# Performance work log

Measured on AMD Instinct MI355X. Metric: run time of the kernel, lower is better.

Reference implementation:

```python
import jax, jax.numpy as jnp
import numpy as np
from jax import lax

D_MODEL = 512; N_HEADS = 32; HEAD_DIM = 16
D_INNER = 1024; D_STATE = 64; HDIM = 64; NH = 16; D_CONV = 4
CONV_CH = D_INNER + 2 * D_STATE          # 1152
D_INPROJ = 2 * D_INNER + 2 * D_STATE + NH  # 2192
B, L = 4, 1024


def setup_inputs() -> dict:
    key = jax.random.key(0)
    ks = jax.random.split(key, 16)
    def rn(k, shape, scale=0.02):
        return jax.random.normal(k, shape, jnp.float32) * scale
    inp = {"h": jax.random.normal(ks[0], (B, L, D_MODEL), jnp.float32)}
    inp["attn_in_w"] = rn(ks[1], (3 * D_MODEL, D_MODEL))
    inp["attn_in_b"] = jnp.zeros((3 * D_MODEL,), jnp.float32)
    inp["attn_out_w"] = rn(ks[2], (D_MODEL, D_MODEL))
    inp["attn_out_b"] = jnp.zeros((D_MODEL,), jnp.float32)
    i = 3
    for p in ("fwd", "bwd"):
        inp[f"{p}_inproj_w"] = rn(ks[i], (D_INPROJ, D_MODEL)); i += 1
        inp[f"{p}_conv_w"] = rn(ks[i], (CONV_CH, D_CONV), 0.1); i += 1
        inp[f"{p}_conv_b"] = jnp.zeros((CONV_CH,), jnp.float32)
        inp[f"{p}_dt_bias"] = rn(ks[i], (NH,), 0.5); i += 1
        inp[f"{p}_A_log"] = jnp.log(jax.random.uniform(ks[i], (NH,), jnp.float32, 1.0, 16.0)); i += 1
        inp[f"{p}_D"] = jnp.ones((NH,), jnp.float32)
        inp[f"{p}_norm_w"] = jnp.ones((D_INNER,), jnp.float32)
        inp[f"{p}_outproj_w"] = rn(ks[i], (D_MODEL, D_INNER)); i += 1
    inp["ln_w"] = jnp.ones((D_MODEL,), jnp.float32)
    inp["ln_b"] = jnp.zeros((D_MODEL,), jnp.float32)
    return inp


def _mha(h, in_w, in_b, out_w, out_b):
    b, l, d = h.shape
    qkv = h @ in_w.T + in_b
    q, k, v = jnp.split(qkv, 3, axis=-1)
    def heads(t):
        return t.reshape(b, l, N_HEADS, HEAD_DIM).transpose(0, 2, 1, 3)
    q, k, v = heads(q), heads(k), heads(v)
    scores = jnp.einsum('bhqd,bhkd->bhqk', q, k) * (1.0 / np.sqrt(HEAD_DIM))
    attn = jax.nn.softmax(scores, axis=-1)
    o = jnp.einsum('bhqk,bhkd->bhqd', attn, v).transpose(0, 2, 1, 3).reshape(b, l, d)
    return o @ out_w.T + out_b


def _causal_dwconv(x, w, bias):
    # x: (b, l, c), w: (c, k) depthwise causal conv
    xt = x.transpose(0, 2, 1)  # (b, c, l)
    out = lax.conv_general_dilated(xt, w[:, None, :], (1,), [(D_CONV - 1, 0)],
                                   feature_group_count=CONV_CH,
                                   dimension_numbers=('NCH', 'OIH', 'NCH'))
    return (out + bias[None, :, None]).transpose(0, 2, 1)


def _ssd(x, dt, A, Bm, Cm):
    # x: (b,l,nh,p), dt: (b,l,nh), Bm/Cm: (b,l,n) (ngroups=1)
    b = x.shape[0]
    dA = jnp.exp(dt * A)          # (b,l,nh)
    dtx = dt[..., None] * x       # (b,l,nh,p)
    def step(hst, inp):
        dA_t, dtx_t, B_t, C_t = inp
        hst = dA_t[:, :, None, None] * hst + dtx_t[..., None] * B_t[:, None, None, :]
        return hst, jnp.einsum('bhpn,bn->bhp', hst, C_t)
    init = jnp.zeros((b, NH, HDIM, D_STATE), x.dtype)
    _, ys = lax.scan(step, init, (dA.transpose(1, 0, 2), dtx.transpose(1, 0, 2, 3),
                                  Bm.transpose(1, 0, 2), Cm.transpose(1, 0, 2)))
    return ys.transpose(1, 0, 2, 3)  # (b,l,nh,p)


def _mamba2(u, inproj_w, conv_w, conv_b, dt_bias, A_log, Dp, norm_w, outproj_w):
    b, l, _ = u.shape
    zxbcdt = u @ inproj_w.T                      # (b,l,2192)
    z = zxbcdt[..., :D_INNER]
    xBC = zxbcdt[..., D_INNER:D_INNER + CONV_CH]
    dt = jax.nn.softplus(zxbcdt[..., D_INNER + CONV_CH:] + dt_bias)  # (b,l,nh)
    xBC = jax.nn.silu(_causal_dwconv(xBC, conv_w, conv_b))
    x = xBC[..., :D_INNER].reshape(b, l, NH, HDIM)
    Bm = xBC[..., D_INNER:D_INNER + D_STATE]
    Cm = xBC[..., D_INNER + D_STATE:]
    A = -jnp.exp(A_log)
    y = _ssd(x, dt, A, Bm, Cm) + Dp[None, None, :, None] * x
    y = y.reshape(b, l, D_INNER) * jax.nn.silu(z)  # gated (norm_before_gate=False)
    y = y * lax.rsqrt(jnp.mean(y * y, axis=-1, keepdims=True) + 1e-5) * norm_w  # RMSNormGated
    return y @ outproj_w.T


def reference(h, attn_in_w, attn_in_b, attn_out_w, attn_out_b,
              fwd_inproj_w, fwd_conv_w, fwd_conv_b, fwd_dt_bias, fwd_A_log, fwd_D, fwd_norm_w, fwd_outproj_w,
              bwd_inproj_w, bwd_conv_w, bwd_conv_b, bwd_dt_bias, bwd_A_log, bwd_D, bwd_norm_w, bwd_outproj_w,
              ln_w, ln_b):
    attn_out = _mha(h, attn_in_w, attn_in_b, attn_out_w, attn_out_b)
    fwd_out = _mamba2(h, fwd_inproj_w, fwd_conv_w, fwd_conv_b, fwd_dt_bias, fwd_A_log, fwd_D, fwd_norm_w, fwd_outproj_w)
    bwd_out = jnp.flip(_mamba2(jnp.flip(h, 1), bwd_inproj_w, bwd_conv_w, bwd_conv_b, bwd_dt_bias, bwd_A_log, bwd_D, bwd_norm_w, bwd_outproj_w), 1)
    s = h + attn_out + fwd_out + bwd_out
    mu = jnp.mean(s, axis=-1, keepdims=True)
    var = jnp.mean((s - mu) ** 2, axis=-1, keepdims=True)
    return (s - mu) * lax.rsqrt(var + 1e-5) * ln_w + ln_b
```

## Files before the change

kernel.cpp:

```cpp
#include <hip/hip_runtime.h>
#include <math.h>
#include <stdint.h>

#define B_ 4
#define L_ 1024
#define DM 512
#define NHA 32
#define HD 16
#define DI 1024
#define DSTATE 64
#define HDIM_ 64
#define NHM 16
#define DCONV 4
#define CONVCH 1152
#define DINPROJ 2192
#define NTOK (B_*L_)
#define QC 64
#define NC (L_/QC)
#define QKVS 5920

typedef __bf16 bf16x8 __attribute__((ext_vector_type(8)));
typedef float f32x4 __attribute__((ext_vector_type(4)));
typedef unsigned short ushort8 __attribute__((ext_vector_type(8)));
typedef unsigned short ushort4v __attribute__((ext_vector_type(4)));
typedef __fp16 fp16x2 __attribute__((ext_vector_type(2)));
typedef _Float16 f16x4 __attribute__((ext_vector_type(4)));
typedef _Float16 f16x8 __attribute__((ext_vector_type(8)));

__device__ __forceinline__ float siluf(float x) {
    return x / (1.0f + __expf(-x));
}

__device__ __forceinline__ unsigned short f2bf(float f) {
    unsigned u = __float_as_uint(f);
    unsigned r = (u + 0x7FFFu + ((u >> 16) & 1u)) >> 16;
    return (unsigned short)r;
}

__device__ __forceinline__ float bf2f(unsigned short u) {
    return __uint_as_float((unsigned)u << 16);
}

__device__ __forceinline__ void cvt8(const float* src, unsigned short* dst) {
    float4 a = ((const float4*)src)[0];
    float4 b = ((const float4*)src)[1];
    ushort8 o;
    o[0] = f2bf(a.x); o[1] = f2bf(a.y); o[2] = f2bf(a.z); o[3] = f2bf(a.w);
    o[4] = f2bf(b.x); o[5] = f2bf(b.y); o[6] = f2bf(b.z); o[7] = f2bf(b.w);
    *(ushort8*)dst = o;
}

__device__ __forceinline__ void gload16(const void* g, void* l) {
    auto gp = reinterpret_cast<const __attribute__((address_space(1))) unsigned int*>(
        reinterpret_cast<uintptr_t>(g));
    auto lp = reinterpret_cast<__attribute__((address_space(3))) unsigned int*>(
        reinterpret_cast<uintptr_t>(l));
    __builtin_amdgcn_global_load_lds(gp, lp, 16, 0, 0);
}

#define S0 262144
#define S1 (S0 + 98304)
#define S2 (S1 + 32768)
#define S3 (S2 + 140288)
#define S4 (S3 + 140288)
__global__ void cvt_all_kernel(const float* __restrict__ h, unsigned short* __restrict__ hB,
                               const float* __restrict__ w1, unsigned short* __restrict__ d1,
                               const float* __restrict__ w2, unsigned short* __restrict__ d2,
                               const float* __restrict__ w3, unsigned short* __restrict__ d3,
                               const float* __restrict__ w4, unsigned short* __restrict__ d4) {
    int i = blockIdx.x * blockDim.x + threadIdx.x;
    const float* src; unsigned short* dst; int off;
    if (i < S0)      { src = h;  dst = hB; off = i; }
    else if (i < S1) { src = w1; dst = d1; off = i - S0; }
    else if (i < S2) { src = w2; dst = d2; off = i - S1; }
    else if (i < S3) { src = w3; dst = d3; off = i - S2; }
    else             { src = w4; dst = d4; off = i - S3; }
    cvt8(src + (size_t)off * 8, dst + (size_t)off * 8);
}

__global__ void cvt_outproj_kernel(const float* __restrict__ fw, const float* __restrict__ bw,
                                   unsigned short* __restrict__ dst) {
    int i = blockIdx.x * blockDim.x + threadIdx.x;
    const int n8 = DM * DI / 8;
    int half = i >= n8;
    int off = half ? i - n8 : i;
    const float* src = half ? bw : fw;
    int e = off * 8;
    int r = e / DI, c = e % DI;
    cvt8(src + e, dst + (size_t)r * 2048 + half * 1024 + c);
}

template <int BN, bool OBF16, bool SWZ>
__global__ __launch_bounds__(256) void gemm_mfma_staged(
        const unsigned short* __restrict__ Ab, const unsigned short* __restrict__ Wb,
        const float* __restrict__ bias, int biasN, void* __restrict__ Cout,
        int M, int N, int K) {
    constexpr int BM = 128, BK = 32;
    constexpr int NF = BN / 32;
    constexpr int BLOADS = BN / 64;
    __shared__ unsigned short As[2][BM * BK];
    __shared__ unsigned short Bs[2][BN * BK];

    const int tid = threadIdx.x;
    const int wave = tid >> 6, lane = tid & 63;
    const int l15 = lane & 15, g = lane >> 4;
    const int wm = wave >> 1, wn = wave & 1;
    int m0, n0;
    if constexpr (SWZ) {
        int d = blockIdx.x;
        int xcd = d & 7, jj = d >> 3;
        n0 = (xcd * 6 + jj % 6) * BN;
        m0 = (jj / 6) * BM;
    } else {
        m0 = blockIdx.y * BM;
        n0 = blockIdx.x * BN;
    }

    f32x4 acc[4][NF];
    #pragma unroll
    for (int mi = 0; mi < 4; ++mi)
        #pragma unroll
        for (int nj = 0; nj < NF; ++nj) acc[mi][nj] = (f32x4){0.f, 0.f, 0.f, 0.f};

    auto stage = [&](int bufi, int k0) {
        #pragma unroll
        for (int i = 0; i < 2; ++i) {
            int c = (wave * 2 + i) * 64 + lane;
            int row = c >> 2;
            int kc = ((c & 3) ^ (row & 3)) * 8;
            gload16(Ab + (size_t)(m0 + row) * K + k0 + kc,
                    &As[bufi][(wave * 2 + i) * 64 * 8]);
        }
        #pragma unroll
        for (int i = 0; i < BLOADS; ++i) {
            int c = (wave * BLOADS + i) * 64 + lane;
            int row = c >> 2;
            int kc = ((c & 3) ^ (row & 3)) * 8;
            int rn = n0 + row; if (rn >= N) rn = N - 1;
            gload16(Wb + (size_t)rn * K + k0 + kc,
                    &Bs[bufi][(wave * BLOADS + i) * 64 * 8]);
        }
    };

    int cur = 0;
    stage(0, 0);
    __syncthreads();
    for (int k0 = 0; k0 < K; k0 += BK) {
        if (k0 + BK < K) stage(cur ^ 1, k0 + BK);
        const unsigned short* Ac = As[cur];
        const unsigned short* Bc = Bs[cur];
        bf16x8 af[4];
        #pragma unroll
        for (int mi = 0; mi < 4; ++mi) {
            int ar = wm * 64 + mi * 16 + l15;
            af[mi] = *(const bf16x8*)(Ac + ar * BK + ((g ^ (ar & 3)) * 8));
        }
        bf16x8 bfr[NF];
        #pragma unroll
        for (int nj = 0; nj < NF; ++nj) {
            int br = wn * (BN / 2) + nj * 16 + l15;
            bfr[nj] = *(const bf16x8*)(Bc + br * BK + ((g ^ (br & 3)) * 8));
        }
        #pragma unroll
        for (int mi = 0; mi < 4; ++mi)
            #pragma unroll
            for (int nj = 0; nj < NF; ++nj)
                acc[mi][nj] = __builtin_amdgcn_mfma_f32_16x16x32_bf16(af[mi], bfr[nj], acc[mi][nj], 0, 0, 0);
        __syncthreads();
        cur ^= 1;
    }

    #pragma unroll
    for (int mi = 0; mi < 4; ++mi) {
        int rbase = m0 + wm * 64 + mi * 16 + g * 4;
        #pragma unroll
        for (int nj = 0; nj < NF; ++nj) {
            int col = n0 + wn * (BN / 2) + nj * 16 + l15;
            if (col < N) {
                float bv = (bias && col < biasN) ? bias[col] : 0.f;
                #pragma unroll
                for (int r = 0; r < 4; ++r) {
                    float v = acc[mi][nj][r] + bv;
                    if constexpr (OBF16)
                        ((unsigned short*)Cout)[(size_t)(rbase + r) * N + col] = f2bf(v);
                    else
                        ((float*)Cout)[(size_t)(rbase + r) * N + col] = v;
                }
            }
        }
    }
}

#define PBAR() do { __builtin_amdgcn_sched_barrier(0); __builtin_amdgcn_s_barrier(); } while (0)
#define MMAQ(MI0, BP, NJ0)                                                                   \
    do {                                                                                     \
        __builtin_amdgcn_s_setprio(1);                                                       \
        _Pragma("unroll")                                                                    \
        for (int i_ = 0; i_ < 4; ++i_) {                                                     \
            _Pragma("unroll")                                                                \
            for (int j_ = 0; j_ < 2; ++j_) {                                                 \
                acc[(MI0)+i_][(NJ0)+j_] = __builtin_amdgcn_mfma_f32_16x16x32_bf16(           \
                    af[i_][0], BP[j_][0], acc[(MI0)+i_][(NJ0)+j_], 0, 0, 0);                 \
                acc[(MI0)+i_][(NJ0)+j_] = __builtin_amdgcn_mfma_f32_16x16x32_bf16(           \
                    af[i_][1], BP[j_][1], acc[(MI0)+i_][(NJ0)+j_], 0, 0, 0);                 \
            }                                                                                \
        }                                                                                    \
        __builtin_amdgcn_s_setprio(0);                                                       \
    } while (0)

__global__ __launch_bounds__(512, 2) void gemm_mega_8phase(
        const unsigned short* __restrict__ Ab, const unsigned short* __restrict__ Wb,
        const float* __restrict__ bias, int biasN, unsigned short* __restrict__ Cout,
        int M, int Nreal, int K) {
    extern __shared__ unsigned short lds[];
    unsigned short* const LA = lds;
    unsigned short* const LB = lds + 4 * 8192;

    const int tid = threadIdx.x;
    const int wave = tid >> 6, lane = tid & 63;
    const int l15 = lane & 15, g4 = lane >> 4;
    const int wm = wave >> 2, wn = wave & 3;

    const int wg = blockIdx.x;
    const int lin = (wg & 7) * 48 + (wg >> 3);
    const int m0 = (lin & 15) * 256;
    const int n0 = (lin >> 4) * 256;

    f32x4 acc[8][4];
    #pragma unroll
    for (int i = 0; i < 8; ++i)
        #pragma unroll
        for (int j = 0; j < 4; ++j) acc[i][j] = (f32x4){0.f, 0.f, 0.f, 0.f};

    auto stA = [&](int buf, int half, int kt) {
        #pragma unroll
        for (int i2 = 0; i2 < 2; ++i2) {
            int c = (wave * 2 + i2) * 64 + lane;
            int row = c >> 3, ch = c & 7;
            gload16(Ab + (size_t)(m0 + half * 128 + row) * K + kt * 64 + ((ch ^ (row & 7)) * 8),
                    LA + (buf * 2 + half) * 8192 + (wave * 2 + i2) * 512);
        }
    };
    auto stB = [&](int buf, int half, int kt) {
        #pragma unroll
        for (int i2 = 0; i2 < 2; ++i2) {
            int c = (wave * 2 + i2) * 64 + lane;
            int row = c >> 3, ch = c & 7;
            int rn = n0 + half * 128 + row;
            if (rn >= Nreal) rn = Nreal - 1;
            gload16(Wb + (size_t)rn * K + kt * 64 + ((ch ^ (row & 7)) * 8),
                    LB + (buf * 2 + half) * 8192 + (wave * 2 + i2) * 512);
        }
    };

    bf16x8 af[4][2], b01[2][2], b23[2][2];

    auto ldA = [&](int buf, int miBase) {
        #pragma unroll
        for (int i = 0; i < 4; ++i) {
            int r = (miBase + i) * 16 + l15;
            #pragma unroll
            for (int ks = 0; ks < 2; ++ks) {
                int ch = ks * 4 + g4;
                af[i][ks] = *(const bf16x8*)(LA + (buf * 2 + wm) * 8192 + r * 64 +
                                             ((ch ^ (r & 7)) * 8));
            }
        }
    };
    auto ldB = [&](int buf, int njBase, bf16x8 (&bp)[2][2]) {
        #pragma unroll
        for (int j = 0; j < 2; ++j) {
            int r = (wn & 1) * 64 + (njBase + j) * 16 + l15;
            #pragma unroll
            for (int ks = 0; ks < 2; ++ks) {
                int ch = ks * 4 + g4;
                bp[j][ks] = *(const bf16x8*)(LB + (buf * 2 + (wn >> 1)) * 8192 + r * 64 +
                                             ((ch ^ (r & 7)) * 8));
            }
        }
    };

    stA(0, 0, 0); stA(0, 1, 0); stB(0, 0, 0); stB(0, 1, 0);
    stB(1, 0, 1); stB(1, 1, 1);
    asm volatile("s_waitcnt vmcnt(4)" ::: "memory");
    PBAR();

    const int NIT = K >> 7;
    for (int it = 0; it < NIT; ++it) {
        const int T1 = 2 * it + 1;
        const bool st = (it + 1 < NIT);
        ldA(0, 0); ldB(0, 0, b01);
        stA(1, 0, T1);
        PBAR();
        MMAQ(0, b01, 0);
        PBAR();
        ldB(0, 2, b23);
        stA(1, 1, T1);
        PBAR();
        MMAQ(0, b23, 2);
        PBAR();
        ldA(0, 4);
        if (st) stB(0, 0, T1 + 1);
        PBAR();
        MMAQ(4, b23, 2);
        PBAR();
        if (st) {
            stB(0, 1, T1 + 1);
            asm volatile("s_waitcnt vmcnt(4)" ::: "memory");
        } else {
            asm volatile("s_waitcnt vmcnt(0)" ::: "memory");
        }
        PBAR();
        MMAQ(4, b01, 0);
        PBAR();
        ldA(1, 0); ldB(1, 0, b01);
        if (st) stA(0, 0, T1 + 1);
        PBAR();
        MMAQ(0, b01, 0);
        PBAR();
        ldB(1, 2, b23);
        if (st) stA(0, 1, T1 + 1);
        PBAR();
        MMAQ(0, b23, 2);
        PBAR();
        ldA(1, 4);
        if (st) stB(1, 0, T1 + 2);
        PBAR();
        MMAQ(4, b23, 2);
        PBAR();
        if (st) {
            stB(1, 1, T1 + 2);
            asm volatile("s_waitcnt vmcnt(4)" ::: "memory");
        }
        PBAR();
        MMAQ(4, b01, 0);
        PBAR();
    }

    #pragma unroll
    for (int mi = 0; mi < 8; ++mi) {
        int rbase = m0 + wm * 128 + mi * 16 + g4 * 4;
        #pragma unroll
        for (int nj = 0; nj < 4; ++nj) {
            int col = n0 + wn * 64 + nj * 16 + l15;
            if (col < Nreal) {
                float bv = (col < biasN) ? bias[col] : 0.f;
                #pragma unroll
                for (int r = 0; r < 4; ++r)
                    Cout[(size_t)(rbase + r) * Nreal + col] = f2bf(acc[mi][nj][r] + bv);
            }
        }
    }
}

#define KP 24
#define VP 132
__global__ __launch_bounds__(256) void attn_mfma_kernel(const unsigned short* __restrict__ qkv,
                                                        unsigned short* __restrict__ ob) {
    const int n = blockIdx.x;
    const int xcd = n & 7;
    const int j = n >> 3;
    const int bh = ((j >> 4) << 3) + xcd;
    const int qt = j & 15;
    const int h = bh & 31;
    const int b = bh >> 5;
    const int tid = threadIdx.x;
    const int wave = tid >> 6, lane = tid & 63;
    const int l15 = lane & 15, g = lane >> 4;

    __shared__ _Float16 Ksm[128 * KP];
    __shared__ _Float16 VsmT[16 * VP];

    const unsigned short* base = qkv + (size_t)b * L_ * QKVS;
    const int qrow = qt * 64 + wave * 16 + l15;

    f16x4 qf;
    {
        ushort4v qv = *(const ushort4v*)(base + (size_t)qrow * QKVS + h * 16 + g * 4);
        fp16x2 qa = __builtin_amdgcn_cvt_pkrtz(bf2f(qv[0]) * 0.25f, bf2f(qv[1]) * 0.25f);
        fp16x2 qb = __builtin_amdgcn_cvt_pkrtz(bf2f(qv[2]) * 0.25f, bf2f(qv[3]) * 0.25f);
        qf[0] = (_Float16)qa[0]; qf[1] = (_Float16)qa[1];
        qf[2] = (_Float16)qb[0]; qf[3] = (_Float16)qb[1];
    }
    f32x4 yacc = (f32x4){0.f, 0.f, 0.f, 0.f};
    float s = 0.f;

    const int sk = tid >> 1;
    const int sd = (tid & 1) * 8;

    for (int c0 = 0; c0 < L_; c0 += 128) {
        {
            ushort8 ka = *(const ushort8*)(base + (size_t)(c0 + sk) * QKVS + 512 + h * 16 + sd);
            fp16x2 k0 = __builtin_amdgcn_cvt_pkrtz(bf2f(ka[0]), bf2f(ka[1]));
            fp16x2 k1 = __builtin_amdgcn_cvt_pkrtz(bf2f(ka[2]), bf2f(ka[3]));
            fp16x2 k2 = __builtin_amdgcn_cvt_pkrtz(bf2f(ka[4]), bf2f(ka[5]));
            fp16x2 k3 = __builtin_amdgcn_cvt_pkrtz(bf2f(ka[6]), bf2f(ka[7]));
            f16x8 kv;
            kv[0] = (_Float16)k0[0]; kv[1] = (_Float16)k0[1];
            kv[2] = (_Float16)k1[0]; kv[3] = (_Float16)k1[1];
            kv[4] = (_Float16)k2[0]; kv[5] = (_Float16)k2[1];
            kv[6] = (_Float16)k3[0]; kv[7] = (_Float16)k3[1];
            *(f16x8*)(&Ksm[sk * KP + sd]) = kv;
            ushort8 va = *(const ushort8*)(base + (size_t)(c0 + sk) * QKVS + 1024 + h * 16 + sd);
            #pragma unroll
            for (int jj = 0; jj < 8; ++jj)
                VsmT[(sd + jj) * VP + sk] = (_Float16)bf2f(va[jj]);
        }
        __syncthreads();
        #pragma unroll
        for (int half = 0; half < 2; ++half) {
            f32x4 st[4];
            #pragma unroll
            for (int ks = 0; ks < 4; ++ks) {
                f16x4 kf = *(const f16x4*)(&Ksm[((half * 4 + ks) * 16 + l15) * KP + g * 4]);
                st[ks] = __builtin_amdgcn_mfma_f32_16x16x16f16(kf, qf, (f32x4){0.f,0.f,0.f,0.f}, 0, 0, 0);
            }
            float p[16];
            float cs = 0.f;
            #pragma unroll
            for (int ks = 0; ks < 4; ++ks) {
                #pragma unroll
                for (int r = 0; r < 4; ++r) {
                    p[ks * 4 + r] = __expf(st[ks][r]);
                    cs += p[ks * 4 + r];
                }
            }
            cs += __shfl_xor(cs, 16);
            cs += __shfl_xor(cs, 32);
            s += cs;
            #pragma unroll
            for (int ks = 0; ks < 4; ++ks) {
                fp16x2 plo = __builtin_amdgcn_cvt_pkrtz(p[ks*4+0], p[ks*4+1]);
                fp16x2 phi = __builtin_amdgcn_cvt_pkrtz(p[ks*4+2], p[ks*4+3]);
                f16x4 pf;
                pf[0] = (_Float16)plo[0]; pf[1] = (_Float16)plo[1];
                pf[2] = (_Float16)phi[0]; pf[3] = (_Float16)phi[1];
                f16x4 vf = *(const f16x4*)(&VsmT[l15 * VP + (half * 4 + ks) * 16 + g * 4]);
                yacc = __builtin_amdgcn_mfma_f32_16x16x16f16(vf, pf, yacc, 0, 0, 0);
            }
        }
        __syncthreads();
    }
    float inv = 1.f / s;
    ushort4v o;
    o[0] = f2bf(yacc[0] * inv);
    o[1] = f2bf(yacc[1] * inv);
    o[2] = f2bf(yacc[2] * inv);
    o[3] = f2bf(yacc[3] * inv);
    *(ushort4v*)(ob + (size_t)(b * L_ + qrow) * 512 + h * 16 + g * 4) = o;
}

__global__ void conv_silu_kernel(const unsigned short* __restrict__ megaA,
                                 const float* __restrict__ cw0, const float* __restrict__ cb0,
                                 const float* __restrict__ cw1, const float* __restrict__ cb1,
                                 unsigned short* __restrict__ out) {
    const int rev = blockIdx.y;
    const float* conv_w = rev ? cw1 : cw0;
    const float* conv_b = rev ? cb1 : cb0;
    int idx = blockIdx.x * blockDim.x + threadIdx.x;
    if (idx >= NTOK * (CONVCH / 4)) return;
    int c4 = (idx % (CONVCH / 4)) * 4;
    int bl = idx / (CONVCH / 4);
    int l = bl % L_;
    int b = bl / L_;
    const unsigned short* src = megaA + (size_t)b * L_ * QKVS + 1536 + rev * DINPROJ + 1024 + c4;
    float4 w0 = *(const float4*)(conv_w + (c4 + 0) * 4);
    float4 w1 = *(const float4*)(conv_w + (c4 + 1) * 4);
    float4 w2 = *(const float4*)(conv_w + (c4 + 2) * 4);
    float4 w3 = *(const float4*)(conv_w + (c4 + 3) * 4);
    float4 acc = *(const float4*)(conv_b + c4);
    const float wt[4][4] = {{w0.x, w0.y, w0.z, w0.w}, {w1.x, w1.y, w1.z, w1.w},
                            {w2.x, w2.y, w2.z, w2.w}, {w3.x, w3.y, w3.z, w3.w}};
    #pragma unroll
    for (int j = 0; j < 4; ++j) {
        int ll = rev ? (l + 3 - j) : (l - 3 + j);
        if (ll >= 0 && ll < L_) {
            ushort4v x = *(const ushort4v*)(src + (size_t)ll * QKVS);
            acc.x = fmaf(wt[0][j], bf2f(x[0]), acc.x);
            acc.y = fmaf(wt[1][j], bf2f(x[1]), acc.y);
            acc.z = fmaf(wt[2][j], bf2f(x[2]), acc.z);
            acc.w = fmaf(wt[3][j], bf2f(x[3]), acc.w);
        }
    }
    ushort4v o;
    o[0] = f2bf(siluf(acc.x)); o[1] = f2bf(siluf(acc.y));
    o[2] = f2bf(siluf(acc.z)); o[3] = f2bf(siluf(acc.w));
    *(ushort4v*)(out + (size_t)rev * NTOK * CONVCH + (size_t)bl * CONVCH + c4) = o;
}

__global__ void dt_exact_kernel(const float* __restrict__ h,
                                const float* __restrict__ wdt0, const float* __restrict__ bias0,
                                const float* __restrict__ wdt1, const float* __restrict__ bias1,
                                float* __restrict__ dt) {
    const int dir = blockIdx.y;
    const float* wdt = dir ? wdt1 : wdt0;
    const float* dbias = dir ? bias1 : bias0;
    const int row = blockIdx.x;
    const int tid = threadIdx.x;
    const int g = tid >> 4, j = tid & 15;
    const float* hr = h + (size_t)row * DM;
    const float* wr = wdt + (size_t)g * DM;
    float s = 0.f;
    #pragma unroll 8
    for (int t = 0; t < 32; ++t) {
        int k = j + t * 16;
        s = fmaf(hr[k], wr[k], s);
    }
    s += __shfl_xor(s, 1); s += __shfl_xor(s, 2);
    s += __shfl_xor(s, 4); s += __shfl_xor(s, 8);
    if (j == 0) {
        float v = s + dbias[g];
        dt[(size_t)dir * NTOK * NHM + (size_t)row * NHM + g] = (v > 20.f) ? v : log1pf(__expf(v));
    }
}

__global__ __launch_bounds__(256) void ssd_chunk_kernel(
        const unsigned short* __restrict__ xbcAll, const float* __restrict__ dtAll,
        const float* __restrict__ Al0, const float* __restrict__ Dp0,
        const float* __restrict__ Al1, const float* __restrict__ Dp1,
        unsigned short* __restrict__ y16, float* __restrict__ Sb0, float* __restrict__ Sb1,
        float* __restrict__ Edec) {
    const int dir = blockIdx.y;
    const int rev = dir;
    const unsigned short* xbc = xbcAll + (size_t)dir * NTOK * CONVCH;
    const float* dtb = dtAll + (size_t)dir * NTOK * NHM;
    float* Sbuf = dir ? Sb1 : Sb0;
    unsigned short* y = y16 + (size_t)dir * NTOK * DI;

    const int bid = blockIdx.x;
    const int q = bid & (NC - 1);
    const int bh = bid / NC;
    const int b = bh >> 4, h = bh & 15;
    const int tid = threadIdx.x;
    const int wave = tid >> 6, lane = tid & 63;
    const int l15 = lane & 15, l4 = lane >> 4;

    __shared__ unsigned short Bn[64 * 72];
    __shared__ unsigned short Cn[64 * 72];
    __shared__ unsigned short Btw[64 * 72];
    __shared__ unsigned short Gt[64 * 72];
    __shared__ unsigned short xT[64 * 72];
    __shared__ float sdt[QC], sc[QC], wsv[QC];

    const float A = -__expf((dir ? Al1 : Al0)[h]);
    const float Dh = (dir ? Dp1 : Dp0)[h];
    const int r = tid >> 2, qq = tid & 3;

    #pragma unroll
    for (int j = 0; j < 4; ++j) {
        int qd = qq + j * 4;
        int t = q * QC + r;
        int l = rev ? (L_ - 1 - t) : t;
        const unsigned short* rowp = xbc + (size_t)(b * L_ + l) * CONVCH;
        *(ushort4v*)&Bn[r * 72 + qd * 4] = *(const ushort4v*)(rowp + 1024 + qd * 4);
        *(ushort4v*)&Cn[r * 72 + qd * 4] = *(const ushort4v*)(rowp + 1088 + qd * 4);
    }
    if (tid < QC) {
        int t = q * QC + tid;
        int l = rev ? (L_ - 1 - t) : t;
        sdt[tid] = dtb[(size_t)(b * L_ + l) * NHM + h];
    }
    __syncthreads();
    if (tid == 0) {
        float run = 0.f;
        for (int i = 0; i < QC; ++i) { run += A * sdt[i]; sc[i] = run; }
    }
    __syncthreads();
    if (tid < QC) wsv[tid] = sdt[tid] * __expf(sc[QC - 1] - sc[tid]);
    if (tid == 0) Edec[dir * 1024 + bid] = __expf(sc[QC - 1]);
    __syncthreads();

    {
        int n = tid >> 2, s0 = (tid & 3) * 16;
        ushort8 o0, o1;
        #pragma unroll
        for (int k = 0; k < 8; ++k) {
            o0[k] = f2bf(bf2f(Bn[(s0 + k) * 72 + n]) * wsv[s0 + k]);
            o1[k] = f2bf(bf2f(Bn[(s0 + 8 + k) * 72 + n]) * wsv[s0 + 8 + k]);
        }
        *(ushort8*)&Btw[n * 72 + s0] = o0;
        *(ushort8*)&Btw[n * 72 + s0 + 8] = o1;
    }
    #pragma unroll
    for (int j = 0; j < 4; ++j) {
        int qd = qq + j * 4;
        int t = q * QC + r;
        int l = rev ? (L_ - 1 - t) : t;
        const unsigned short* rowp = xbc + (size_t)(b * L_ + l) * CONVCH + h * 64;
        ushort4v xv = *(const ushort4v*)(rowp + qd * 4);
        xT[(qd * 4 + 0) * 72 + r] = xv[0];
        xT[(qd * 4 + 1) * 72 + r] = xv[1];
        xT[(qd * 4 + 2) * 72 + r] = xv[2];
        xT[(qd * 4 + 3) * 72 + r] = xv[3];
    }
    __syncthreads();

    f32x4 accG[4];
    #pragma unroll
    for (int j = 0; j < 4; ++j) accG[j] = (f32x4){0.f, 0.f, 0.f, 0.f};
    #pragma unroll
    for (int k0 = 0; k0 < 64; k0 += 32) {
        bf16x8 af = *(const bf16x8*)&Bn[(wave * 16 + l15) * 72 + l4 * 8 + k0];
        #pragma unroll
        for (int j = 0; j < 4; ++j) {
            bf16x8 bfj = *(const bf16x8*)&Cn[(j * 16 + l15) * 72 + l4 * 8 + k0];
            accG[j] = __builtin_amdgcn_mfma_f32_16x16x32_bf16(af, bfj, accG[j], 0, 0, 0);
        }
    }
    #pragma unroll
    for (int j = 0; j < 4; ++j) {
        #pragma unroll
        for (int rr = 0; rr < 4; ++rr) {
            int s = wave * 16 + l4 * 4 + rr;
            int i = j * 16 + l15;
            float g = (s <= i) ? accG[j][rr] * sdt[s] * __expf(sc[i] - sc[s]) : 0.f;
            Gt[i * 72 + s] = f2bf(g);
        }
    }
    __syncthreads();

    {
        f32x4 accY[4];
        #pragma unroll
        for (int j = 0; j < 4; ++j) accY[j] = (f32x4){0.f, 0.f, 0.f, 0.f};
        #pragma unroll
        for (int k0 = 0; k0 < 64; k0 += 32) {
            bf16x8 af = *(const bf16x8*)&Gt[(wave * 16 + l15) * 72 + l4 * 8 + k0];
            #pragma unroll
            for (int j = 0; j < 4; ++j) {
                bf16x8 bfj = *(const bf16x8*)&xT[(j * 16 + l15) * 72 + l4 * 8 + k0];
                accY[j] = __builtin_amdgcn_mfma_f32_16x16x32_bf16(af, bfj, accY[j], 0, 0, 0);
            }
        }
        #pragma unroll
        for (int j = 0; j < 4; ++j) {
            #pragma unroll
            for (int rr = 0; rr < 4; ++rr) {
                int i = wave * 16 + l4 * 4 + rr;
                int p = j * 16 + l15;
                int t = q * QC + i;
                int l = rev ? (L_ - 1 - t) : t;
                float xv = bf2f(xT[p * 72 + i]);
                y[(size_t)(b * L_ + l) * DI + h * 64 + p] = f2bf(accY[j][rr] + Dh * xv);
            }
        }
    }
    {
        f32x4 accS[4];
        #pragma unroll
        for (int j = 0; j < 4; ++j) accS[j] = (f32x4){0.f, 0.f, 0.f, 0.f};
        #pragma unroll
        for (int k0 = 0; k0 < 64; k0 += 32) {
            bf16x8 af = *(const bf16x8*)&xT[(wave * 16 + l15) * 72 + l4 * 8 + k0];
            #pragma unroll
            for (int j = 0; j < 4; ++j) {
                bf16x8 bfj = *(const bf16x8*)&Btw[(j * 16 + l15) * 72 + l4 * 8 + k0];
                accS[j] = __builtin_amdgcn_mfma_f32_16x16x32_bf16(af, bfj, accS[j], 0, 0, 0);
            }
        }
        float* Sq = Sbuf + (size_t)bid * 4096;
        #pragma unroll
        for (int j = 0; j < 4; ++j) {
            #pragma unroll
            for (int rr = 0; rr < 4; ++rr) {
                int p = wave * 16 + l4 * 4 + rr;
                int n = j * 16 + l15;
                Sq[p * 64 + n] = accS[j][rr];
            }
        }
    }
}

__global__ void ssd_chain_kernel(float* __restrict__ Sb0, float* __restrict__ Sb1,
                                 const float* __restrict__ Edec) {
    const int dir = blockIdx.z;
    float* Sbuf = dir ? Sb1 : Sb0;
    const int bh = blockIdx.x;
    const int e = blockIdx.y * 256 + threadIdx.x;
    float* base = Sbuf + (size_t)bh * NC * 4096 + e;
    const float* Ep = Edec + dir * 1024 + bh * NC;
    float hst = 0.f;
    float tmp = base[0];
    #pragma unroll
    for (int q = 0; q < NC; ++q) {
        float nxt = (q + 1 < NC) ? base[(size_t)(q + 1) * 4096] : 0.f;
        float E = Ep[q];
        base[(size_t)q * 4096] = hst;
        hst = fmaf(E, hst, tmp);
        tmp = nxt;
    }
}

__global__ __launch_bounds__(256) void ssd_corr_kernel(
        const unsigned short* __restrict__ xbcAll, const float* __restrict__ dtAll,
        const float* __restrict__ Al0, const float* __restrict__ Al1,
        const float* __restrict__ Sb0, const float* __restrict__ Sb1,
        unsigned short* __restrict__ y16) {
    const int dir = blockIdx.y;
    const int rev = dir;
    const unsigned short* xbc = xbcAll + (size_t)dir * NTOK * CONVCH;
    const float* dtb = dtAll + (size_t)dir * NTOK * NHM;
    const float* Sbuf = dir ? Sb1 : Sb0;
    unsigned short* y = y16 + (size_t)dir * NTOK * DI;

    const int bid = blockIdx.x;
    const int q = bid & (NC - 1);
    const int bh = bid / NC;
    const int b = bh >> 4, h = bh & 15;
    const int tid = threadIdx.x;
    const int wave = tid >> 6, lane = tid & 63;
    const int l15 = lane & 15, l4 = lane >> 4;

    __shared__ unsigned short Cb[64 * 72];
    __shared__ unsigned short Hb[64 * 72];
    __shared__ float sdt[QC], sc[QC];
    const float A = -__expf((dir ? Al1 : Al0)[h]);
    const int r = tid >> 2, qq = tid & 3;
    const float* Sq = Sbuf + (size_t)bid * 4096;

    #pragma unroll
    for (int j = 0; j < 4; ++j) {
        int qd = qq + j * 4;
        int t = q * QC + r;
        int l = rev ? (L_ - 1 - t) : t;
        const unsigned short* rowp = xbc + (size_t)(b * L_ + l) * CONVCH;
        *(ushort4v*)&Cb[r * 72 + qd * 4] = *(const ushort4v*)(rowp + 1088 + qd * 4);
        float4 hv = ((const float4*)Sq)[r * 16 + qd];
        ushort4v hh;
        hh[0] = f2bf(hv.x); hh[1] = f2bf(hv.y); hh[2] = f2bf(hv.z); hh[3] = f2bf(hv.w);
        *(ushort4v*)&Hb[r * 72 + qd * 4] = hh;
    }
    if (tid < QC) {
        int t = q * QC + tid;
        int l = rev ? (L_ - 1 - t) : t;
        sdt[tid] = dtb[(size_t)(b * L_ + l) * NHM + h];
    }
    __syncthreads();
    if (tid == 0) {
        float run = 0.f;
        for (int i = 0; i < QC; ++i) { run += A * sdt[i]; sc[i] = run; }
    }
    __syncthreads();

    f32x4 acc[4];
    #pragma unroll
    for (int j = 0; j < 4; ++j) acc[j] = (f32x4){0.f, 0.f, 0.f, 0.f};
    #pragma unroll
    for (int k0 = 0; k0 < 64; k0 += 32) {
        bf16x8 af = *(const bf16x8*)&Cb[(wave * 16 + l15) * 72 + l4 * 8 + k0];
        #pragma unroll
        for (int j = 0; j < 4; ++j) {
            bf16x8 bfj = *(const bf16x8*)&Hb[(j * 16 + l15) * 72 + l4 * 8 + k0];
            acc[j] = __builtin_amdgcn_mfma_f32_16x16x32_bf16(af, bfj, acc[j], 0, 0, 0);
        }
    }
    #pragma unroll
    for (int j = 0; j < 4; ++j) {
        #pragma unroll
        for (int rr = 0; rr < 4; ++rr) {
            int i = wave * 16 + l4 * 4 + rr;
            int p = j * 16 + l15;
            int t = q * QC + i;
            int l = rev ? (L_ - 1 - t) : t;
            float e = __expf(sc[i]);
            unsigned short* yp = &y[(size_t)(b * L_ + l) * DI + h * 64 + p];
            *yp = f2bf(bf2f(*yp) + e * acc[j][rr]);
        }
    }
}

__global__ void gate_rmsnorm_kernel(const unsigned short* __restrict__ y16,
                                    const unsigned short* __restrict__ megaA,
                                    const float* __restrict__ nw0, const float* __restrict__ nw1,
                                    unsigned short* __restrict__ yb) {
    const int dir = blockIdx.y;
    const float* norm_w = dir ? nw1 : nw0;
    const int row = blockIdx.x;
    const int tid = threadIdx.x;
    const unsigned short* z = megaA + (size_t)row * QKVS + 1536 + dir * DINPROJ;
    const unsigned short* yr = y16 + (size_t)dir * NTOK * DI + (size_t)row * DI;
    float v[4];
    float ss = 0.f;
    #pragma unroll
    for (int i = 0; i < 4; ++i) {
        int c = i * 256 + tid;
        float g = siluf(bf2f(z[c]));
        v[i] = bf2f(yr[c]) * g;
        ss = fmaf(v[i], v[i], ss);
    }
    #pragma unroll
    for (int off = 32; off > 0; off >>= 1) ss += __shfl_xor(ss, off);
    __shared__ float red[4];
    int wid = tid >> 6, lane = tid & 63;
    if (lane == 0) red[wid] = ss;
    __syncthreads();
    ss = red[0] + red[1] + red[2] + red[3];
    float scale = rsqrtf(ss * (1.0f / 1024.0f) + 1e-5f);
    #pragma unroll
    for (int i = 0; i < 4; ++i) {
        int c = i * 256 + tid;
        yb[(size_t)row * 2048 + dir * 1024 + c] = f2bf(v[i] * scale * norm_w[c]);
    }
}

__global__ void final_ln_kernel(const float* __restrict__ h, const float* __restrict__ attn,
                                const float* __restrict__ msum,
                                const float* __restrict__ ln_w, const float* __restrict__ ln_b,
                                float* __restrict__ out) {
    const int row = blockIdx.x;
    const int tid = threadIdx.x;
    size_t base = (size_t)row * DM;
    float v[2];
    float sum = 0.f, sq = 0.f;
    #pragma unroll
    for (int i = 0; i < 2; ++i) {
        int c = i * 256 + tid;
        float s = h[base + c] + attn[base + c] + msum[base + c];
        v[i] = s;
        sum += s;
        sq = fmaf(s, s, sq);
    }
    #pragma unroll
    for (int off = 32; off > 0; off >>= 1) {
        sum += __shfl_xor(sum, off);
        sq += __shfl_xor(sq, off);
    }
    __shared__ float rsum[4], rsq[4];
    int wid = tid >> 6, lane = tid & 63;
    if (lane == 0) { rsum[wid] = sum; rsq[wid] = sq; }
    __syncthreads();
    sum = rsum[0] + rsum[1] + rsum[2] + rsum[3];
    sq = rsq[0] + rsq[1] + rsq[2] + rsq[3];
    float mu = sum * (1.0f / DM);
    float var = sq * (1.0f / DM) - mu * mu;
    float rs = rsqrtf(var + 1e-5f);
    #pragma unroll
    for (int i = 0; i < 2; ++i) {
        int c = i * 256 + tid;
        out[base + c] = (v[i] - mu) * rs * ln_w[c] + ln_b[c];
    }
}

extern "C" void kernel_launch(void* const* d_in, const int* in_sizes, int n_in,
                              void* d_out, int out_size, void* d_ws, size_t ws_size,
                              hipStream_t stream) {
    const float* h          = (const float*)d_in[0];
    const float* attn_in_w  = (const float*)d_in[1];
    const float* attn_in_b  = (const float*)d_in[2];
    const float* attn_out_w = (const float*)d_in[3];
    const float* attn_out_b = (const float*)d_in[4];
    const float* ln_w       = (const float*)d_in[21];
    const float* ln_b       = (const float*)d_in[22];
    float* out = (float*)d_out;

    float* ws = (float*)d_ws;
    unsigned short* megaA = (unsigned short*)ws;
    unsigned short* bufXBC = (unsigned short*)(ws + 12124160);
    float* bufDT   = ws + 12124160 + 4718592;
    float* bufY    = bufDT + 131072;
    float* bufATTN = bufY + 4194304;
    float* gateReg = bufATTN + 2097152;
    float* sReg    = gateReg + 4194304;
    float* bufEdec = sReg + 4194304;
    unsigned short* hB = (unsigned short*)(bufEdec + 2048);
    unsigned short* wBIG   = (unsigned short*)gateReg;
    unsigned short* wAOUT  = wBIG + (size_t)QKVS * DM;
    unsigned short* gatedB = (unsigned short*)gateReg;
    unsigned short* actB   = (unsigned short*)sReg;
    float* bufS0           = sReg;
    float* bufS1           = gateReg;
    unsigned short* wC     = (unsigned short*)sReg;
    unsigned short* y16    = (unsigned short*)bufY;
    float* msum            = bufY;

    const float* inproj_fwd = (const float*)d_in[5];
    const float* inproj_bwd = (const float*)d_in[13];

    dim3 blk(256);

    cvt_all_kernel<<<dim3(S4 / 256), blk, 0, stream>>>(
        h, hB, attn_in_w, wBIG, attn_out_w, wAOUT,
        inproj_fwd, wBIG + (size_t)1536 * DM, inproj_bwd, wBIG + (size_t)3728 * DM);

    static bool smemSet = false;
    if (!smemSet) {
        (void)hipFuncSetAttribute(reinterpret_cast<const void*>(gemm_mega_8phase),
                                  hipFuncAttributeMaxDynamicSharedMemorySize, 131072);
        smemSet = true;
    }
    gemm_mega_8phase<<<dim3(16 * 24), dim3(512), 131072, stream>>>(
        hB, wBIG, attn_in_b, 1536, megaA, NTOK, QKVS, DM);

    attn_mfma_kernel<<<dim3(B_ * NHA * (L_ / 64)), blk, 0, stream>>>(megaA, actB);
    gemm_mfma_staged<64, false, false><<<dim3(DM / 64, NTOK / 128), blk, 0, stream>>>(
        actB, wAOUT, attn_out_b, DM, bufATTN, NTOK, DM, DM);

    dt_exact_kernel<<<dim3(NTOK, 2), blk, 0, stream>>>(
        h, inproj_fwd + (size_t)(DINPROJ - NHM) * DM, (const float*)d_in[8],
        inproj_bwd + (size_t)(DINPROJ - NHM) * DM, (const float*)d_in[16], bufDT);
    conv_silu_kernel<<<dim3((NTOK * (CONVCH / 4) + 255) / 256, 2), blk, 0, stream>>>(
        megaA, (const float*)d_in[6], (const float*)d_in[7],
        (const float*)d_in[14], (const float*)d_in[15], bufXBC);

    ssd_chunk_kernel<<<dim3(B_ * NHM * NC, 2), blk, 0, stream>>>(
        bufXBC, bufDT, (const float*)d_in[9], (const float*)d_in[10],
        (const float*)d_in[17], (const float*)d_in[18], y16, bufS0, bufS1, bufEdec);
    ssd_chain_kernel<<<dim3(B_ * NHM, 16, 2), blk, 0, stream>>>(bufS0, bufS1, bufEdec);
    ssd_corr_kernel<<<dim3(B_ * NHM * NC, 2), blk, 0, stream>>>(
        bufXBC, bufDT, (const float*)d_in[9], (const float*)d_in[17], bufS0, bufS1, y16);
    gate_rmsnorm_kernel<<<dim3(NTOK, 2), blk, 0, stream>>>(
        y16, megaA, (const float*)d_in[11], (const float*)d_in[19], gatedB);

    cvt_outproj_kernel<<<dim3((2 * DM * DI / 8 + 255) / 256), blk, 0, stream>>>(
        (const float*)d_in[12], (const float*)d_in[20], wC);
    gemm_mfma_staged<64, false, false><<<dim3(DM / 64, NTOK / 128), blk, 0, stream>>>(
        gatedB, wC, nullptr, 0, msum, NTOK, DM, 2048);

    final_ln_kernel<<<dim3(NTOK), blk, 0, stream>>>(
        h, bufATTN, msum, ln_w, ln_b, out);
}
```

Baseline: 245.6 us.

## Split-K the out-projection GEMM, fuse dt directions, and tweak LDS swizzle and barriers

```diff
diff --git a/kernel.cpp b/kernel.cpp
--- a/kernel.cpp
+++ b/kernel.cpp
@@ -56,6 +56,10 @@
     auto lp = reinterpret_cast<__attribute__((address_space(3))) unsigned int*>(
         reinterpret_cast<uintptr_t>(l));
     __builtin_amdgcn_global_load_lds(gp, lp, 16, 0, 0);
+}
+
+__device__ __forceinline__ int swz3(int row) {
+    return (row ^ (row >> 2)) & 3;
 }
 
 #define S0 262144
@@ -90,108 +94,6 @@
     cvt8(src + e, dst + (size_t)r * 2048 + half * 1024 + c);
 }
 
-template <int BN, bool OBF16, bool SWZ>
-__global__ __launch_bounds__(256) void gemm_mfma_staged(
-        const unsigned short* __restrict__ Ab, const unsigned short* __restrict__ Wb,
-        const float* __restrict__ bias, int biasN, void* __restrict__ Cout,
-        int M, int N, int K) {
-    constexpr int BM = 128, BK = 32;
-    constexpr int NF = BN / 32;
-    constexpr int BLOADS = BN / 64;
-    __shared__ unsigned short As[2][BM * BK];
-    __shared__ unsigned short Bs[2][BN * BK];
-
-    const int tid = threadIdx.x;
-    const int wave = tid >> 6, lane = tid & 63;
-    const int l15 = lane & 15, g = lane >> 4;
-    const int wm = wave >> 1, wn = wave & 1;
-    int m0, n0;
-    if constexpr (SWZ) {
-        int d = blockIdx.x;
-        int xcd = d & 7, jj = d >> 3;
-        n0 = (xcd * 6 + jj % 6) * BN;
-        m0 = (jj / 6) * BM;
-    } else {
-        m0 = blockIdx.y * BM;
-        n0 = blockIdx.x * BN;
-    }
-
-    f32x4 acc[4][NF];
-    #pragma unroll
-    for (int mi = 0; mi < 4; ++mi)
-        #pragma unroll
-        for (int nj = 0; nj < NF; ++nj) acc[mi][nj] = (f32x4){0.f, 0.f, 0.f, 0.f};
-
-    auto stage = [&](int bufi, int k0) {
-        #pragma unroll
-        for (int i = 0; i < 2; ++i) {
-            int c = (wave * 2 + i) * 64 + lane;
-            int row = c >> 2;
-            int kc = ((c & 3) ^ (row & 3)) * 8;
-            gload16(Ab + (size_t)(m0 + row) * K + k0 + kc,
-                    &As[bufi][(wave * 2 + i) * 64 * 8]);
-        }
-        #pragma unroll
-        for (int i = 0; i < BLOADS; ++i) {
-            int c = (wave * BLOADS + i) * 64 + lane;
-            int row = c >> 2;
-            int kc = ((c & 3) ^ (row & 3)) * 8;
-            int rn = n0 + row; if (rn >= N) rn = N - 1;
-            gload16(Wb + (size_t)rn * K + k0 + kc,
-                    &Bs[bufi][(wave * BLOADS + i) * 64 * 8]);
-        }
-    };
-
-    int cur = 0;
-    stage(0, 0);
-    __syncthreads();
-    for (int k0 = 0; k0 < K; k0 += BK) {
-        if (k0 + BK < K) stage(cur ^ 1, k0 + BK);
-        const unsigned short* Ac = As[cur];
-        const unsigned short* Bc = Bs[cur];
-        bf16x8 af[4];
-        #pragma unroll
-        for (int mi = 0; mi < 4; ++mi) {
-            int ar = wm * 64 + mi * 16 + l15;
-            af[mi] = *(const bf16x8*)(Ac + ar * BK + ((g ^ (ar & 3)) * 8));
-        }
-        bf16x8 bfr[NF];
-        #pragma unroll
-        for (int nj = 0; nj < NF; ++nj) {
-            int br = wn * (BN / 2) + nj * 16 + l15;
-            bfr[nj] = *(const bf16x8*)(Bc + br * BK + ((g ^ (br & 3)) * 8));
-        }
-        #pragma unroll
-        for (int mi = 0; mi < 4; ++mi)
-            #pragma unroll
-            for (int nj = 0; nj < NF; ++nj)
-                acc[mi][nj] = __builtin_amdgcn_mfma_f32_16x16x32_bf16(af[mi], bfr[nj], acc[mi][nj], 0, 0, 0);
-        __syncthreads();
-        cur ^= 1;
-    }
-
-    #pragma unroll
-    for (int mi = 0; mi < 4; ++mi) {
-        int rbase = m0 + wm * 64 + mi * 16 + g * 4;
-        #pragma unroll
-        for (int nj = 0; nj < NF; ++nj) {
-            int col = n0 + wn * (BN / 2) + nj * 16 + l15;
-            if (col < N) {
-                float bv = (bias && col < biasN) ? bias[col] : 0.f;
-                #pragma unroll
-                for (int r = 0; r < 4; ++r) {
-                    float v = acc[mi][nj][r] + bv;
-                    if constexpr (OBF16)
-                        ((unsigned short*)Cout)[(size_t)(rbase + r) * N + col] = f2bf(v);
-                    else
-                        ((float*)Cout)[(size_t)(rbase + r) * N + col] = v;
-                }
-            }
-        }
-    }
-}
-
-#define PBAR() do { __builtin_amdgcn_sched_barrier(0); __builtin_amdgcn_s_barrier(); } while (0)
 #define MMAQ(MI0, BP, NJ0)                                                                   \
     do {                                                                                     \
         __builtin_amdgcn_s_setprio(1);                                                       \
@@ -207,6 +109,7 @@
         }                                                                                    \
         __builtin_amdgcn_s_setprio(0);                                                       \
     } while (0)
+#define BAR() __builtin_amdgcn_s_barrier()
 
 __global__ __launch_bounds__(512, 2) void gemm_mega_8phase(
         const unsigned short* __restrict__ Ab, const unsigned short* __restrict__ Wb,
@@ -283,7 +186,7 @@
     stA(0, 0, 0); stA(0, 1, 0); stB(0, 0, 0); stB(0, 1, 0);
     stB(1, 0, 1); stB(1, 1, 1);
     asm volatile("s_waitcnt vmcnt(4)" ::: "memory");
-    PBAR();
+    BAR();
 
     const int NIT = K >> 7;
     for (int it = 0; it < NIT; ++it) {
@@ -291,50 +194,50 @@
         const bool st = (it + 1 < NIT);
         ldA(0, 0); ldB(0, 0, b01);
         stA(1, 0, T1);
-        PBAR();
+        BAR();
         MMAQ(0, b01, 0);
-        PBAR();
+        BAR();
         ldB(0, 2, b23);
         stA(1, 1, T1);
-        PBAR();
+        BAR();
         MMAQ(0, b23, 2);
-        PBAR();
+        BAR();
         ldA(0, 4);
         if (st) stB(0, 0, T1 + 1);
-        PBAR();
+        BAR();
         MMAQ(4, b23, 2);
-        PBAR();
+        BAR();
         if (st) {
             stB(0, 1, T1 + 1);
             asm volatile("s_waitcnt vmcnt(4)" ::: "memory");
         } else {
             asm volatile("s_waitcnt vmcnt(0)" ::: "memory");
         }
-        PBAR();
+        BAR();
         MMAQ(4, b01, 0);
-        PBAR();
+        BAR();
         ldA(1, 0); ldB(1, 0, b01);
         if (st) stA(0, 0, T1 + 1);
-        PBAR();
+        BAR();
         MMAQ(0, b01, 0);
-        PBAR();
+        BAR();
         ldB(1, 2, b23);
         if (st) stA(0, 1, T1 + 1);
-        PBAR();
+        BAR();
         MMAQ(0, b23, 2);
-        PBAR();
+        BAR();
         ldA(1, 4);
         if (st) stB(1, 0, T1 + 2);
-        PBAR();
+        BAR();
         MMAQ(4, b23, 2);
-        PBAR();
+        BAR();
         if (st) {
             stB(1, 1, T1 + 2);
             asm volatile("s_waitcnt vmcnt(4)" ::: "memory");
         }
-        PBAR();
+        BAR();
         MMAQ(4, b01, 0);
-        PBAR();
+        BAR();
     }
 
     #pragma unroll
@@ -348,6 +251,113 @@
                 #pragma unroll
                 for (int r = 0; r < 4; ++r)
                     Cout[(size_t)(rbase + r) * Nreal + col] = f2bf(acc[mi][nj][r] + bv);
+            }
+        }
+    }
+}
+
+template <int BN, bool OBF16, bool SWZ, bool SPLITK>
+__global__ __launch_bounds__(256, 4) void gemm_mfma_staged(
+        const unsigned short* __restrict__ Ab, const unsigned short* __restrict__ Wb,
+        const float* __restrict__ bias, int biasN, void* __restrict__ Cout,
+        int M, int N, int K) {
+    constexpr int BM = 128, BK = 32;
+    constexpr int NF = BN / 32;
+    constexpr int BLOADS = BN / 64;
+    __shared__ unsigned short As[2][BM * BK];
+    __shared__ unsigned short Bs[2][BN * BK];
+
+    const int tid = threadIdx.x;
+    const int wave = tid >> 6, lane = tid & 63;
+    const int l15 = lane & 15, g = lane >> 4;
+    const int wm = wave >> 1, wn = wave & 1;
+    int m0, n0;
+    if constexpr (SWZ) {
+        int d = blockIdx.x;
+        int xcd = d & 7, jj = d >> 3;
+        n0 = (xcd * 6 + jj % 6) * BN;
+        m0 = (jj / 6) * BM;
+    } else {
+        m0 = blockIdx.y * BM;
+        n0 = blockIdx.x * BN;
+    }
+
+    f32x4 acc[4][NF];
+    #pragma unroll
+    for (int mi = 0; mi < 4; ++mi)
+        #pragma unroll
+        for (int nj = 0; nj < NF; ++nj) acc[mi][nj] = (f32x4){0.f, 0.f, 0.f, 0.f};
+
+    auto stage = [&](int bufi, int k0) {
+        #pragma unroll
+        for (int i = 0; i < 2; ++i) {
+            int c = (wave * 2 + i) * 64 + lane;
+            int row = c >> 2;
+            int kc = ((c & 3) ^ swz3(row)) * 8;
+            gload16(Ab + (size_t)(m0 + row) * K + k0 + kc,
+                    &As[bufi][(wave * 2 + i) * 64 * 8]);
+        }
+        #pragma unroll
+        for (int i = 0; i < BLOADS; ++i) {
+            int c = (wave * BLOADS + i) * 64 + lane;
+            int row = c >> 2;
+            int kc = ((c & 3) ^ swz3(row)) * 8;
+            int rn = n0 + row; if (rn >= N) rn = N - 1;
+            gload16(Wb + (size_t)rn * K + k0 + kc,
+                    &Bs[bufi][(wave * BLOADS + i) * 64 * 8]);
+        }
+    };
+
+    const int kBeg = SPLITK ? blockIdx.z * (K >> 1) : 0;
+    const int kLen = SPLITK ? (K >> 1) : K;
+
+    int cur = 0;
+    stage(0, kBeg);
+    __syncthreads();
+    for (int kk = 0; kk < kLen; kk += BK) {
+        if (kk + BK < kLen) stage(cur ^ 1, kBeg + kk + BK);
+        const unsigned short* Ac = As[cur];
+        const unsigned short* Bc = Bs[cur];
+        bf16x8 af[4];
+        #pragma unroll
+        for (int mi = 0; mi < 4; ++mi) {
+            int ar = wm * 64 + mi * 16 + l15;
+            af[mi] = *(const bf16x8*)(Ac + ar * BK + ((g ^ swz3(ar)) * 8));
+        }
+        bf16x8 bfr[NF];
+        #pragma unroll
+        for (int nj = 0; nj < NF; ++nj) {
+            int br = wn * (BN / 2) + nj * 16 + l15;
+            bfr[nj] = *(const bf16x8*)(Bc + br * BK + ((g ^ swz3(br)) * 8));
+        }
+        #pragma unroll
+        for (int mi = 0; mi < 4; ++mi)
+            #pragma unroll
+            for (int nj = 0; nj < NF; ++nj)
+                acc[mi][nj] = __builtin_amdgcn_mfma_f32_16x16x32_bf16(af[mi], bfr[nj], acc[mi][nj], 0, 0, 0);
+        __syncthreads();
+        cur ^= 1;
+    }
+
+    float* CoutF = (float*)Cout;
+    if constexpr (SPLITK) CoutF += (size_t)blockIdx.z * M * N;
+
+    #pragma unroll
+    for (int mi = 0; mi < 4; ++mi) {
+        int rbase = m0 + wm * 64 + mi * 16 + g * 4;
+        #pragma unroll
+        for (int nj = 0; nj < NF; ++nj) {
+            int col = n0 + wn * (BN / 2) + nj * 16 + l15;
+            if (col < N) {
+                float bv = (bias && col < biasN && (!SPLITK || blockIdx.z == 0)) ? bias[col] : 0.f;
+                #pragma unroll
+                for (int r = 0; r < 4; ++r) {
+                    float v = acc[mi][nj][r] + bv;
+                    if constexpr (OBF16)
+                        ((unsigned short*)Cout)[(size_t)(rbase + r) * N + col] = f2bf(v);
+                    else
+                        CoutF[(size_t)(rbase + r) * N + col] = v;
+                }
             }
         }
     }
@@ -492,25 +502,29 @@
                                 const float* __restrict__ wdt0, const float* __restrict__ bias0,
                                 const float* __restrict__ wdt1, const float* __restrict__ bias1,
                                 float* __restrict__ dt) {
-    const int dir = blockIdx.y;
-    const float* wdt = dir ? wdt1 : wdt0;
-    const float* dbias = dir ? bias1 : bias0;
     const int row = blockIdx.x;
     const int tid = threadIdx.x;
     const int g = tid >> 4, j = tid & 15;
     const float* hr = h + (size_t)row * DM;
-    const float* wr = wdt + (size_t)g * DM;
-    float s = 0.f;
+    const float* wr0 = wdt0 + (size_t)g * DM;
+    const float* wr1 = wdt1 + (size_t)g * DM;
+    float s0 = 0.f, s1 = 0.f;
     #pragma unroll 8
     for (int t = 0; t < 32; ++t) {
         int k = j + t * 16;
-        s = fmaf(hr[k], wr[k], s);
-    }
-    s += __shfl_xor(s, 1); s += __shfl_xor(s, 2);
-    s += __shfl_xor(s, 4); s += __shfl_xor(s, 8);
+        float hv = hr[k];
+        s0 = fmaf(hv, wr0[k], s0);
+        s1 = fmaf(hv, wr1[k], s1);
+    }
+    s0 += __shfl_xor(s0, 1); s0 += __shfl_xor(s0, 2);
+    s0 += __shfl_xor(s0, 4); s0 += __shfl_xor(s0, 8);
+    s1 += __shfl_xor(s1, 1); s1 += __shfl_xor(s1, 2);
+    s1 += __shfl_xor(s1, 4); s1 += __shfl_xor(s1, 8);
     if (j == 0) {
-        float v = s + dbias[g];
-        dt[(size_t)dir * NTOK * NHM + (size_t)row * NHM + g] = (v > 20.f) ? v : log1pf(__expf(v));
+        float v0 = s0 + bias0[g];
+        float v1 = s1 + bias1[g];
+        dt[(size_t)row * NHM + g] = (v0 > 20.f) ? v0 : log1pf(__expf(v0));
+        dt[(size_t)NTOK * NHM + (size_t)row * NHM + g] = (v1 > 20.f) ? v1 : log1pf(__expf(v1));
     }
 }
 
@@ -804,7 +818,7 @@
 }
 
 __global__ void final_ln_kernel(const float* __restrict__ h, const float* __restrict__ attn,
-                                const float* __restrict__ msum,
+                                const float* __restrict__ msum, const float* __restrict__ msum2,
                                 const float* __restrict__ ln_w, const float* __restrict__ ln_b,
                                 float* __restrict__ out) {
     const int row = blockIdx.x;
@@ -815,7 +829,7 @@
     #pragma unroll
     for (int i = 0; i < 2; ++i) {
         int c = i * 256 + tid;
-        float s = h[base + c] + attn[base + c] + msum[base + c];
+        float s = h[base + c] + attn[base + c] + msum[base + c] + msum2[base + c];
         v[i] = s;
         sum += s;
         sq = fmaf(s, s, sq);
@@ -872,6 +886,7 @@
     unsigned short* wC     = (unsigned short*)sReg;
     unsigned short* y16    = (unsigned short*)bufY;
     float* msum            = bufY;
+    float* msum2           = bufY + (size_t)NTOK * DM;
 
     const float* inproj_fwd = (const float*)d_in[5];
     const float* inproj_bwd = (const float*)d_in[13];
@@ -892,10 +907,10 @@
         hB, wBIG, attn_in_b, 1536, megaA, NTOK, QKVS, DM);
 
     attn_mfma_kernel<<<dim3(B_ * NHA * (L_ / 64)), blk, 0, stream>>>(megaA, actB);
-    gemm_mfma_staged<64, false, false><<<dim3(DM / 64, NTOK / 128), blk, 0, stream>>>(
+    gemm_mfma_staged<64, false, false, false><<<dim3(DM / 64, NTOK / 128), blk, 0, stream>>>(
         actB, wAOUT, attn_out_b, DM, bufATTN, NTOK, DM, DM);
 
-    dt_exact_kernel<<<dim3(NTOK, 2), blk, 0, stream>>>(
+    dt_exact_kernel<<<dim3(NTOK), blk, 0, stream>>>(
         h, inproj_fwd + (size_t)(DINPROJ - NHM) * DM, (const float*)d_in[8],
         inproj_bwd + (size_t)(DINPROJ - NHM) * DM, (const float*)d_in[16], bufDT);
     conv_silu_kernel<<<dim3((NTOK * (CONVCH / 4) + 255) / 256, 2), blk, 0, stream>>>(
@@ -913,9 +928,9 @@
 
     cvt_outproj_kernel<<<dim3((2 * DM * DI / 8 + 255) / 256), blk, 0, stream>>>(
         (const float*)d_in[12], (const float*)d_in[20], wC);
-    gemm_mfma_staged<64, false, false><<<dim3(DM / 64, NTOK / 128), blk, 0, stream>>>(
+    gemm_mfma_staged<64, false, false, true><<<dim3(DM / 64, NTOK / 128, 2), blk, 0, stream>>>(
         gatedB, wC, nullptr, 0, msum, NTOK, DM, 2048);
 
     final_ln_kernel<<<dim3(NTOK), blk, 0, stream>>>(
-        h, bufATTN, msum, ln_w, ln_b, out);
-}
+        h, bufATTN, msum, msum2, ln_w, ln_b, out);
+}
```

Result: no change. 241.9 us (-1.5%).
